# Optimization experiments

Measured on AMD Instinct MI355X. Metric: run time of the kernel, lower is better.

Reference implementation:

```python
import jax, jax.numpy as jnp
import numpy as np

EPS_LN = 1e-6
EPS_COS = 1e-8  # torch F.cosine_similarity default eps


def setup_inputs() -> dict:
    key = jax.random.key(0)
    ks = jax.random.split(key, 6)
    in_dim, hidden, out_dim, b = 1024, 512, 128, 8192
    x = jax.random.normal(ks[0], (b, in_dim), dtype=jnp.float32)
    # Linear layers: torch default init ~ U(-1/sqrt(fan_in), 1/sqrt(fan_in))
    w1 = jax.random.uniform(ks[1], (in_dim, hidden), jnp.float32, -1, 1) / np.sqrt(in_dim)
    b1 = jax.random.uniform(ks[2], (hidden,), jnp.float32, -1, 1) / np.sqrt(in_dim)
    w2 = jax.random.uniform(ks[3], (hidden, out_dim), jnp.float32, -1, 1) / np.sqrt(hidden)
    b2 = jax.random.uniform(ks[4], (out_dim,), jnp.float32, -1, 1) / np.sqrt(hidden)
    prelu_a = jnp.float32(0.25)  # nn.PReLU default: single shared parameter, init 0.25
    ln_gamma = jnp.ones((hidden,), jnp.float32)
    ln_beta = jnp.zeros((hidden,), jnp.float32)
    return {"x": x, "w1": w1, "b1": b1, "prelu_a": prelu_a,
            "ln_gamma": ln_gamma, "ln_beta": ln_beta, "w2": w2, "b2": b2}


def _layer_norm(h, gamma, beta):
    mu = jnp.mean(h, axis=-1, keepdims=True)
    var = jnp.mean(jnp.square(h - mu), axis=-1, keepdims=True)
    return (h - mu) * jax.lax.rsqrt(var + EPS_LN) * gamma + beta


def reference(x, w1, b1, prelu_a, ln_gamma, ln_beta, w2, b2):
    h = x @ w1 + b1                              # [b, hidden]
    h = jnp.where(h >= 0, h, prelu_a * h)        # PReLU
    h = _layer_norm(h, ln_gamma, ln_beta)        # Dropout is identity in reference
    z = h @ w2 + b2                              # [b, out_dim]
    # get_y_hat: full pairwise cosine similarity as normalize + Gram matmul
    norms = jnp.maximum(jnp.linalg.norm(z, axis=1, keepdims=True), EPS_COS)
    zn = z / norms                               # [b, out_dim]
    y_hat = zn @ zn.T                            # [b, b]
    return z, y_hat
```

## Files before the change

### kernel.cpp

```cpp
#include <hip/hip_runtime.h>
#include <stdint.h>

typedef uint16_t u16;
typedef __bf16 bf16x8 __attribute__((ext_vector_type(8)));
typedef float f32x4 __attribute__((ext_vector_type(4)));

__device__ __forceinline__ u16 f2bf(float f) {
  union { float f; uint32_t u; } v; v.f = f;
  uint32_t u = v.u;
  u += 0x7FFFu + ((u >> 16) & 1u);
  return (u16)(u >> 16);
}
__device__ __forceinline__ float bf2f(u16 h) {
  union { uint32_t u; float f; } v; v.u = ((uint32_t)h) << 16; return v.f;
}

__global__ void transpose_f32_to_bf16(const float* __restrict__ in,
                                      u16* __restrict__ out, int R, int C) {
  __shared__ float tile[32][33];
  int bx = blockIdx.x * 32, by = blockIdx.y * 32;
  int tx = threadIdx.x, ty = threadIdx.y;
  for (int i = 0; i < 32; i += 8)
    tile[ty + i][tx] = in[(size_t)(by + ty + i) * C + bx + tx];
  __syncthreads();
  for (int i = 0; i < 32; i += 8)
    out[(size_t)(bx + ty + i) * R + by + tx] = f2bf(tile[tx][ty + i]);
}

#define BM 128
#define BN 128
#define BKT 64

__launch_bounds__(256)
__global__ void gemm1_kernel(const float* __restrict__ A,
                             const u16* __restrict__ Bt,
                             const float* __restrict__ bias,
                             const float* __restrict__ prelu_a,
                             u16* __restrict__ out) {
  const int N = 512, K = 1024;
  __shared__ u16 As[BM][BKT + 8];
  __shared__ u16 Bs[BN][BKT + 8];
  const int lane = threadIdx.x & 63, wave = threadIdx.x >> 6;
  const int row0 = blockIdx.x * BM, col0 = blockIdx.y * BN;

  f32x4 zero4 = {0.f, 0.f, 0.f, 0.f};
  f32x4 acc[2][8];
  for (int i = 0; i < 2; ++i)
    for (int j = 0; j < 8; ++j) acc[i][j] = zero4;

  for (int k0 = 0; k0 < K; k0 += BKT) {
    for (int s = 0; s < 4; ++s) {
      int c = threadIdx.x + s * 256;
      int r = c >> 3, kc = (c & 7) << 3;
      const float4* p = (const float4*)(A + (size_t)(row0 + r) * K + k0 + kc);
      float4 f0 = p[0], f1 = p[1];
      u16 tmp[8] = {f2bf(f0.x), f2bf(f0.y), f2bf(f0.z), f2bf(f0.w),
                    f2bf(f1.x), f2bf(f1.y), f2bf(f1.z), f2bf(f1.w)};
      *(uint4*)(&As[r][kc]) = *(uint4*)tmp;
      *(uint4*)(&Bs[r][kc]) = *(const uint4*)(Bt + (size_t)(col0 + r) * K + k0 + kc);
    }
    __syncthreads();
    for (int kk = 0; kk < BKT; kk += 32) {
      bf16x8 a[2], b[8];
      for (int i = 0; i < 2; ++i)
        a[i] = *(const bf16x8*)(&As[wave * 32 + i * 16 + (lane & 15)][kk + (lane >> 4) * 8]);
      for (int j = 0; j < 8; ++j)
        b[j] = *(const bf16x8*)(&Bs[j * 16 + (lane & 15)][kk + (lane >> 4) * 8]);
      for (int i = 0; i < 2; ++i)
        for (int j = 0; j < 8; ++j)
          acc[i][j] = __builtin_amdgcn_mfma_f32_16x16x32_bf16(a[i], b[j], acc[i][j], 0, 0, 0);
    }
    __syncthreads();
  }

  float ap = *prelu_a;
  for (int i = 0; i < 2; ++i)
    for (int r = 0; r < 4; ++r) {
      int row = row0 + wave * 32 + i * 16 + (lane >> 4) * 4 + r;
      for (int j = 0; j < 8; ++j) {
        int col = col0 + j * 16 + (lane & 15);
        float v = acc[i][j][r] + bias[col];
        v = v >= 0.f ? v : ap * v;
        out[(size_t)row * N + col] = f2bf(v);
      }
    }
}

__launch_bounds__(256)
__global__ void ln_kernel(const u16* __restrict__ h, const float* __restrict__ gamma,
                          const float* __restrict__ beta, u16* __restrict__ out) {
  int lane = threadIdx.x & 63, wave = threadIdx.x >> 6;
  int row = blockIdx.x * 4 + wave;
  uint4 raw = *(const uint4*)(h + (size_t)row * 512 + lane * 8);
  u16* up = (u16*)&raw;
  float v[8], s = 0.f, s2 = 0.f;
  for (int e = 0; e < 8; ++e) { v[e] = bf2f(up[e]); s += v[e]; s2 += v[e] * v[e]; }
  for (int m = 1; m < 64; m <<= 1) { s += __shfl_xor(s, m); s2 += __shfl_xor(s2, m); }
  float mu = s * (1.f / 512.f);
  float var = s2 * (1.f / 512.f) - mu * mu;
  float rstd = rsqrtf(var + 1e-6f);
  u16 o[8];
  for (int e = 0; e < 8; ++e) {
    int c = lane * 8 + e;
    o[e] = f2bf((v[e] - mu) * rstd * gamma[c] + beta[c]);
  }
  *(uint4*)(out + (size_t)row * 512 + lane * 8) = *(uint4*)o;
}

__launch_bounds__(256)
__global__ void gemm2_kernel(const u16* __restrict__ A, const u16* __restrict__ Bt,
                             const float* __restrict__ bias,
                             float* __restrict__ z, u16* __restrict__ zn) {
  const int K = 512;
  __shared__ u16 As[BM][BKT + 8];
  __shared__ u16 Bs[BN][BKT + 8];
  const int lane = threadIdx.x & 63, wave = threadIdx.x >> 6;
  const int row0 = blockIdx.x * BM;

  f32x4 zero4 = {0.f, 0.f, 0.f, 0.f};
  f32x4 acc[2][8];
  for (int i = 0; i < 2; ++i)
    for (int j = 0; j < 8; ++j) acc[i][j] = zero4;

  for (int k0 = 0; k0 < K; k0 += BKT) {
    for (int s = 0; s < 4; ++s) {
      int c = threadIdx.x + s * 256;
      int r = c >> 3, kc = (c & 7) << 3;
      *(uint4*)(&As[r][kc]) = *(const uint4*)(A + (size_t)(row0 + r) * K + k0 + kc);
      *(uint4*)(&Bs[r][kc]) = *(const uint4*)(Bt + (size_t)r * K + k0 + kc);
    }
    __syncthreads();
    for (int kk = 0; kk < BKT; kk += 32) {
      bf16x8 a[2], b[8];
      for (int i = 0; i < 2; ++i)
        a[i] = *(const bf16x8*)(&As[wave * 32 + i * 16 + (lane & 15)][kk + (lane >> 4) * 8]);
      for (int j = 0; j < 8; ++j)
        b[j] = *(const bf16x8*)(&Bs[j * 16 + (lane & 15)][kk + (lane >> 4) * 8]);
      for (int i = 0; i < 2; ++i)
        for (int j = 0; j < 8; ++j)
          acc[i][j] = __builtin_amdgcn_mfma_f32_16x16x32_bf16(a[i], b[j], acc[i][j], 0, 0, 0);
    }
    __syncthreads();
  }

  for (int i = 0; i < 2; ++i)
    for (int r = 0; r < 4; ++r) {
      int row = row0 + wave * 32 + i * 16 + (lane >> 4) * 4 + r;
      float vv[8], s = 0.f;
      for (int j = 0; j < 8; ++j) {
        int col = j * 16 + (lane & 15);
        float v = acc[i][j][r] + bias[col];
        vv[j] = v; s += v * v;
      }
      s += __shfl_xor(s, 1); s += __shfl_xor(s, 2);
      s += __shfl_xor(s, 4); s += __shfl_xor(s, 8);
      float inv = 1.f / fmaxf(sqrtf(s), 1e-8f);
      for (int j = 0; j < 8; ++j) {
        int col = j * 16 + (lane & 15);
        z[(size_t)row * 128 + col] = vv[j];
        zn[(size_t)row * 128 + col] = f2bf(vv[j] * inv);
      }
    }
}

__launch_bounds__(256)
__global__ void gram_kernel(const u16* __restrict__ Z, float* __restrict__ y) {
  const int K = 128, Bdim = 8192;
  __shared__ u16 As[BM][BKT + 8];
  __shared__ u16 Bs[BN][BKT + 8];
  const int lane = threadIdx.x & 63, wave = threadIdx.x >> 6;
  const int row0 = blockIdx.x * BM, col0 = blockIdx.y * BN;

  f32x4 zero4 = {0.f, 0.f, 0.f, 0.f};
  f32x4 acc[2][8];
  for (int i = 0; i < 2; ++i)
    for (int j = 0; j < 8; ++j) acc[i][j] = zero4;

  for (int k0 = 0; k0 < K; k0 += BKT) {
    for (int s = 0; s < 4; ++s) {
      int c = threadIdx.x + s * 256;
      int r = c >> 3, kc = (c & 7) << 3;
      *(uint4*)(&As[r][kc]) = *(const uint4*)(Z + (size_t)(row0 + r) * K + k0 + kc);
      *(uint4*)(&Bs[r][kc]) = *(const uint4*)(Z + (size_t)(col0 + r) * K + k0 + kc);
    }
    __syncthreads();
    for (int kk = 0; kk < BKT; kk += 32) {
      bf16x8 a[2], b[8];
      for (int i = 0; i < 2; ++i)
        a[i] = *(const bf16x8*)(&As[wave * 32 + i * 16 + (lane & 15)][kk + (lane >> 4) * 8]);
      for (int j = 0; j < 8; ++j)
        b[j] = *(const bf16x8*)(&Bs[j * 16 + (lane & 15)][kk + (lane >> 4) * 8]);
      for (int i = 0; i < 2; ++i)
        for (int j = 0; j < 8; ++j)
          acc[i][j] = __builtin_amdgcn_mfma_f32_16x16x32_bf16(a[i], b[j], acc[i][j], 0, 0, 0);
    }
    __syncthreads();
  }

  for (int i = 0; i < 2; ++i)
    for (int r = 0; r < 4; ++r) {
      int row = row0 + wave * 32 + i * 16 + (lane >> 4) * 4 + r;
      for (int j = 0; j < 8; ++j) {
        int col = col0 + j * 16 + (lane & 15);
        y[(size_t)row * Bdim + col] = acc[i][j][r];
      }
    }
}

extern "C" void kernel_launch(void* const* d_in, const int* in_sizes, int n_in,
                              void* d_out, int out_size, void* d_ws, size_t ws_size,
                              hipStream_t stream) {
  const float* x       = (const float*)d_in[0];
  const float* w1      = (const float*)d_in[1];
  const float* b1      = (const float*)d_in[2];
  const float* prelu_a = (const float*)d_in[3];
  const float* gamma   = (const float*)d_in[4];
  const float* beta    = (const float*)d_in[5];
  const float* w2      = (const float*)d_in[6];
  const float* b2      = (const float*)d_in[7];

  float* z_out = (float*)d_out;
  float* yhat  = z_out + (size_t)8192 * 128;

  char* ws = (char*)d_ws;
  u16* w1t  = (u16*)(ws);
  u16* w2t  = (u16*)(ws + (1u << 20));
  u16* hact = (u16*)(ws + (1u << 20) + (1u << 17));
  u16* hln  = (u16*)(ws + (1u << 20) + (1u << 17) + (8u << 20));
  u16* zn   = (u16*)(ws + (1u << 20) + (1u << 17) + (16u << 20));

  transpose_f32_to_bf16<<<dim3(16, 32), dim3(32, 8), 0, stream>>>(w1, w1t, 1024, 512);
  transpose_f32_to_bf16<<<dim3(4, 16), dim3(32, 8), 0, stream>>>(w2, w2t, 512, 128);
  gemm1_kernel<<<dim3(64, 4), 256, 0, stream>>>(x, w1t, b1, prelu_a, hact);
  ln_kernel<<<2048, 256, 0, stream>>>(hact, gamma, beta, hln);
  gemm2_kernel<<<64, 256, 0, stream>>>(hln, w2t, b2, z_out, zn);
  gram_kernel<<<dim3(64, 64), 256, 0, stream>>>(zn, yhat);
}
```

Before: 367.6 us.

## Fuse LayerNorm into GEMM1, merge transposes, single-stage gram, nontemporal stores

Folds the LayerNorm into the first GEMM by giving each block 32 full rows across all 512 hidden columns and reducing row statistics through shared memory. This removes the intermediate activation round-trip and one launch. It also merges the two weight transposes into a single launch. The gram kernel now loads the whole K=128 slice at once, dropping its k-loop syncs, and the large y_hat and z outputs use nontemporal stores. GEMM1 now reloads all of W1 per 32-row block and uses a much larger shared tile, which may reduce occupancy.

```diff
diff --git a/kernel.cpp b/kernel.cpp
--- a/kernel.cpp
+++ b/kernel.cpp
@@ -15,8 +15,14 @@
   union { uint32_t u; float f; } v; v.u = ((uint32_t)h) << 16; return v.f;
 }
 
-__global__ void transpose_f32_to_bf16(const float* __restrict__ in,
-                                      u16* __restrict__ out, int R, int C) {
+__global__ void transpose_both(const float* __restrict__ w1, u16* __restrict__ w1t,
+                               const float* __restrict__ w2, u16* __restrict__ w2t) {
+  const float* in; u16* out; int R, C;
+  if (blockIdx.z == 0) { in = w1; out = w1t; R = 1024; C = 512; }
+  else {
+    if (blockIdx.x >= 4 || blockIdx.y >= 16) return;
+    in = w2; out = w2t; R = 512; C = 128;
+  }
   __shared__ float tile[32][33];
   int bx = blockIdx.x * 32, by = blockIdx.y * 32;
   int tx = threadIdx.x, ty = threadIdx.y;
@@ -27,85 +33,130 @@
     out[(size_t)(bx + ty + i) * R + by + tx] = f2bf(tile[tx][ty + i]);
 }
 
+#define G1_BK 64
+
+__launch_bounds__(256)
+__global__ void gemm1_ln_kernel(const float* __restrict__ A,
+                                const u16* __restrict__ Bt,
+                                const float* __restrict__ bias,
+                                const float* __restrict__ prelu_a,
+                                const float* __restrict__ gamma,
+                                const float* __restrict__ beta,
+                                u16* __restrict__ out) {
+  const int K = 1024, N = 512;
+  __shared__ u16 As[32][G1_BK + 8];
+  __shared__ u16 Bs[512][G1_BK + 8];
+  const int lane = threadIdx.x & 63, wave = threadIdx.x >> 6;
+  const int row0 = blockIdx.x * 32;
+
+  f32x4 zero4 = {0.f, 0.f, 0.f, 0.f};
+  f32x4 acc[2][8];
+#pragma unroll
+  for (int i = 0; i < 2; ++i)
+#pragma unroll
+    for (int j = 0; j < 8; ++j) acc[i][j] = zero4;
+
+  const int r0 = threadIdx.x >> 3, kc0 = (threadIdx.x & 7) << 3;
+
+  for (int k0 = 0; k0 < K; k0 += G1_BK) {
+    {
+      const float4* p = (const float4*)(A + (size_t)(row0 + r0) * K + k0 + kc0);
+      float4 f0 = p[0], f1 = p[1];
+      u16 tmp[8] = {f2bf(f0.x), f2bf(f0.y), f2bf(f0.z), f2bf(f0.w),
+                    f2bf(f1.x), f2bf(f1.y), f2bf(f1.z), f2bf(f1.w)};
+      *(uint4*)(&As[r0][kc0]) = *(uint4*)tmp;
+    }
+#pragma unroll
+    for (int s = 0; s < 16; ++s) {
+      int r = r0 + s * 32;
+      *(uint4*)(&Bs[r][kc0]) = *(const uint4*)(Bt + (size_t)r * K + k0 + kc0);
+    }
+    __syncthreads();
+#pragma unroll
+    for (int kk = 0; kk < G1_BK; kk += 32) {
+      bf16x8 a[2], b[8];
+#pragma unroll
+      for (int i = 0; i < 2; ++i)
+        a[i] = *(const bf16x8*)(&As[i * 16 + (lane & 15)][kk + (lane >> 4) * 8]);
+#pragma unroll
+      for (int j = 0; j < 8; ++j)
+        b[j] = *(const bf16x8*)(&Bs[wave * 128 + j * 16 + (lane & 15)][kk + (lane >> 4) * 8]);
+#pragma unroll
+      for (int i = 0; i < 2; ++i)
+#pragma unroll
+        for (int j = 0; j < 8; ++j)
+          acc[i][j] = __builtin_amdgcn_mfma_f32_16x16x32_bf16(a[i], b[j], acc[i][j], 0, 0, 0);
+    }
+    __syncthreads();
+  }
+
+  float ap = *prelu_a;
+  float bcol[8], gcol[8], btc[8];
+#pragma unroll
+  for (int j = 0; j < 8; ++j) {
+    int col = wave * 128 + j * 16 + (lane & 15);
+    bcol[j] = bias[col]; gcol[j] = gamma[col]; btc[j] = beta[col];
+  }
+
+  float s1[2][4], s2[2][4];
+#pragma unroll
+  for (int i = 0; i < 2; ++i)
+#pragma unroll
+    for (int r = 0; r < 4; ++r) {
+      float s = 0.f, q = 0.f;
+#pragma unroll
+      for (int j = 0; j < 8; ++j) {
+        float v = acc[i][j][r] + bcol[j];
+        v = v >= 0.f ? v : ap * v;
+        acc[i][j][r] = v;
+        s += v; q += v * v;
+      }
+      s += __shfl_xor(s, 1); q += __shfl_xor(q, 1);
+      s += __shfl_xor(s, 2); q += __shfl_xor(q, 2);
+      s += __shfl_xor(s, 4); q += __shfl_xor(q, 4);
+      s += __shfl_xor(s, 8); q += __shfl_xor(q, 8);
+      s1[i][r] = s; s2[i][r] = q;
+    }
+
+  float* red = (float*)&As[0][0];
+  if ((lane & 15) == 0) {
+#pragma unroll
+    for (int i = 0; i < 2; ++i)
+#pragma unroll
+      for (int r = 0; r < 4; ++r) {
+        int row = i * 16 + (lane >> 4) * 4 + r;
+        red[(row * 4 + wave) * 2 + 0] = s1[i][r];
+        red[(row * 4 + wave) * 2 + 1] = s2[i][r];
+      }
+  }
+  __syncthreads();
+
+#pragma unroll
+  for (int i = 0; i < 2; ++i)
+#pragma unroll
+    for (int r = 0; r < 4; ++r) {
+      int row = i * 16 + (lane >> 4) * 4 + r;
+      float S = 0.f, Q = 0.f;
+#pragma unroll
+      for (int w = 0; w < 4; ++w) {
+        S += red[(row * 4 + w) * 2 + 0];
+        Q += red[(row * 4 + w) * 2 + 1];
+      }
+      float mu = S * (1.f / 512.f);
+      float var = Q * (1.f / 512.f) - mu * mu;
+      float rstd = rsqrtf(var + 1e-6f);
+#pragma unroll
+      for (int j = 0; j < 8; ++j) {
+        int col = wave * 128 + j * 16 + (lane & 15);
+        out[(size_t)(row0 + row) * N + col] =
+            f2bf((acc[i][j][r] - mu) * rstd * gcol[j] + btc[j]);
+      }
+    }
+}
+
 #define BM 128
 #define BN 128
 #define BKT 64
-
-__launch_bounds__(256)
-__global__ void gemm1_kernel(const float* __restrict__ A,
-                             const u16* __restrict__ Bt,
-                             const float* __restrict__ bias,
-                             const float* __restrict__ prelu_a,
-                             u16* __restrict__ out) {
-  const int N = 512, K = 1024;
-  __shared__ u16 As[BM][BKT + 8];
-  __shared__ u16 Bs[BN][BKT + 8];
-  const int lane = threadIdx.x & 63, wave = threadIdx.x >> 6;
-  const int row0 = blockIdx.x * BM, col0 = blockIdx.y * BN;
-
-  f32x4 zero4 = {0.f, 0.f, 0.f, 0.f};
-  f32x4 acc[2][8];
-  for (int i = 0; i < 2; ++i)
-    for (int j = 0; j < 8; ++j) acc[i][j] = zero4;
-
-  for (int k0 = 0; k0 < K; k0 += BKT) {
-    for (int s = 0; s < 4; ++s) {
-      int c = threadIdx.x + s * 256;
-      int r = c >> 3, kc = (c & 7) << 3;
-      const float4* p = (const float4*)(A + (size_t)(row0 + r) * K + k0 + kc);
-      float4 f0 = p[0], f1 = p[1];
-      u16 tmp[8] = {f2bf(f0.x), f2bf(f0.y), f2bf(f0.z), f2bf(f0.w),
-                    f2bf(f1.x), f2bf(f1.y), f2bf(f1.z), f2bf(f1.w)};
-      *(uint4*)(&As[r][kc]) = *(uint4*)tmp;
-      *(uint4*)(&Bs[r][kc]) = *(const uint4*)(Bt + (size_t)(col0 + r) * K + k0 + kc);
-    }
-    __syncthreads();
-    for (int kk = 0; kk < BKT; kk += 32) {
-      bf16x8 a[2], b[8];
-      for (int i = 0; i < 2; ++i)
-        a[i] = *(const bf16x8*)(&As[wave * 32 + i * 16 + (lane & 15)][kk + (lane >> 4) * 8]);
-      for (int j = 0; j < 8; ++j)
-        b[j] = *(const bf16x8*)(&Bs[j * 16 + (lane & 15)][kk + (lane >> 4) * 8]);
-      for (int i = 0; i < 2; ++i)
-        for (int j = 0; j < 8; ++j)
-          acc[i][j] = __builtin_amdgcn_mfma_f32_16x16x32_bf16(a[i], b[j], acc[i][j], 0, 0, 0);
-    }
-    __syncthreads();
-  }
-
-  float ap = *prelu_a;
-  for (int i = 0; i < 2; ++i)
-    for (int r = 0; r < 4; ++r) {
-      int row = row0 + wave * 32 + i * 16 + (lane >> 4) * 4 + r;
-      for (int j = 0; j < 8; ++j) {
-        int col = col0 + j * 16 + (lane & 15);
-        float v = acc[i][j][r] + bias[col];
-        v = v >= 0.f ? v : ap * v;
-        out[(size_t)row * N + col] = f2bf(v);
-      }
-    }
-}
-
-__launch_bounds__(256)
-__global__ void ln_kernel(const u16* __restrict__ h, const float* __restrict__ gamma,
-                          const float* __restrict__ beta, u16* __restrict__ out) {
-  int lane = threadIdx.x & 63, wave = threadIdx.x >> 6;
-  int row = blockIdx.x * 4 + wave;
-  uint4 raw = *(const uint4*)(h + (size_t)row * 512 + lane * 8);
-  u16* up = (u16*)&raw;
-  float v[8], s = 0.f, s2 = 0.f;
-  for (int e = 0; e < 8; ++e) { v[e] = bf2f(up[e]); s += v[e]; s2 += v[e] * v[e]; }
-  for (int m = 1; m < 64; m <<= 1) { s += __shfl_xor(s, m); s2 += __shfl_xor(s2, m); }
-  float mu = s * (1.f / 512.f);
-  float var = s2 * (1.f / 512.f) - mu * mu;
-  float rstd = rsqrtf(var + 1e-6f);
-  u16 o[8];
-  for (int e = 0; e < 8; ++e) {
-    int c = lane * 8 + e;
-    o[e] = f2bf((v[e] - mu) * rstd * gamma[c] + beta[c]);
-  }
-  *(uint4*)(out + (size_t)row * 512 + lane * 8) = *(uint4*)o;
-}
 
 __launch_bounds__(256)
 __global__ void gemm2_kernel(const u16* __restrict__ A, const u16* __restrict__ Bt,
@@ -119,34 +170,46 @@
 
   f32x4 zero4 = {0.f, 0.f, 0.f, 0.f};
   f32x4 acc[2][8];
-  for (int i = 0; i < 2; ++i)
+#pragma unroll
+  for (int i = 0; i < 2; ++i)
+#pragma unroll
     for (int j = 0; j < 8; ++j) acc[i][j] = zero4;
 
+  const int r0 = threadIdx.x >> 3, kc0 = (threadIdx.x & 7) << 3;
+
   for (int k0 = 0; k0 < K; k0 += BKT) {
+#pragma unroll
     for (int s = 0; s < 4; ++s) {
-      int c = threadIdx.x + s * 256;
-      int r = c >> 3, kc = (c & 7) << 3;
-      *(uint4*)(&As[r][kc]) = *(const uint4*)(A + (size_t)(row0 + r) * K + k0 + kc);
-      *(uint4*)(&Bs[r][kc]) = *(const uint4*)(Bt + (size_t)r * K + k0 + kc);
+      int r = r0 + s * 32;
+      *(uint4*)(&As[r][kc0]) = *(const uint4*)(A + (size_t)(row0 + r) * K + k0 + kc0);
+      *(uint4*)(&Bs[r][kc0]) = *(const uint4*)(Bt + (size_t)r * K + k0 + kc0);
     }
     __syncthreads();
+#pragma unroll
     for (int kk = 0; kk < BKT; kk += 32) {
       bf16x8 a[2], b[8];
+#pragma unroll
       for (int i = 0; i < 2; ++i)
         a[i] = *(const bf16x8*)(&As[wave * 32 + i * 16 + (lane & 15)][kk + (lane >> 4) * 8]);
+#pragma unroll
       for (int j = 0; j < 8; ++j)
         b[j] = *(const bf16x8*)(&Bs[j * 16 + (lane & 15)][kk + (lane >> 4) * 8]);
+#pragma unroll
       for (int i = 0; i < 2; ++i)
+#pragma unroll
         for (int j = 0; j < 8; ++j)
           acc[i][j] = __builtin_amdgcn_mfma_f32_16x16x32_bf16(a[i], b[j], acc[i][j], 0, 0, 0);
     }
     __syncthreads();
   }
 
-  for (int i = 0; i < 2; ++i)
+#pragma unroll
+  for (int i = 0; i < 2; ++i)
+#pragma unroll
     for (int r = 0; r < 4; ++r) {
       int row = row0 + wave * 32 + i * 16 + (lane >> 4) * 4 + r;
       float vv[8], s = 0.f;
+#pragma unroll
       for (int j = 0; j < 8; ++j) {
         int col = j * 16 + (lane & 15);
         float v = acc[i][j][r] + bias[col];
@@ -155,9 +218,10 @@
       s += __shfl_xor(s, 1); s += __shfl_xor(s, 2);
       s += __shfl_xor(s, 4); s += __shfl_xor(s, 8);
       float inv = 1.f / fmaxf(sqrtf(s), 1e-8f);
+#pragma unroll
       for (int j = 0; j < 8; ++j) {
         int col = j * 16 + (lane & 15);
-        z[(size_t)row * 128 + col] = vv[j];
+        __builtin_nontemporal_store(vv[j], &z[(size_t)row * 128 + col]);
         zn[(size_t)row * 128 + col] = f2bf(vv[j] * inv);
       }
     }
@@ -166,43 +230,52 @@
 __launch_bounds__(256)
 __global__ void gram_kernel(const u16* __restrict__ Z, float* __restrict__ y) {
   const int K = 128, Bdim = 8192;
-  __shared__ u16 As[BM][BKT + 8];
-  __shared__ u16 Bs[BN][BKT + 8];
+  __shared__ u16 As[128][K + 8];
+  __shared__ u16 Bs[128][K + 8];
   const int lane = threadIdx.x & 63, wave = threadIdx.x >> 6;
-  const int row0 = blockIdx.x * BM, col0 = blockIdx.y * BN;
+  const int row0 = blockIdx.x * 128, col0 = blockIdx.y * 128;
 
   f32x4 zero4 = {0.f, 0.f, 0.f, 0.f};
   f32x4 acc[2][8];
-  for (int i = 0; i < 2; ++i)
+#pragma unroll
+  for (int i = 0; i < 2; ++i)
+#pragma unroll
     for (int j = 0; j < 8; ++j) acc[i][j] = zero4;
 
-  for (int k0 = 0; k0 < K; k0 += BKT) {
-    for (int s = 0; s < 4; ++s) {
-      int c = threadIdx.x + s * 256;
-      int r = c >> 3, kc = (c & 7) << 3;
-      *(uint4*)(&As[r][kc]) = *(const uint4*)(Z + (size_t)(row0 + r) * K + k0 + kc);
-      *(uint4*)(&Bs[r][kc]) = *(const uint4*)(Z + (size_t)(col0 + r) * K + k0 + kc);
-    }
-    __syncthreads();
-    for (int kk = 0; kk < BKT; kk += 32) {
-      bf16x8 a[2], b[8];
-      for (int i = 0; i < 2; ++i)
-        a[i] = *(const bf16x8*)(&As[wave * 32 + i * 16 + (lane & 15)][kk + (lane >> 4) * 8]);
+  const int r0 = threadIdx.x >> 4, kc0 = (threadIdx.x & 15) << 3;
+#pragma unroll
+  for (int s = 0; s < 8; ++s) {
+    int r = r0 + s * 16;
+    *(uint4*)(&As[r][kc0]) = *(const uint4*)(Z + (size_t)(row0 + r) * K + kc0);
+    *(uint4*)(&Bs[r][kc0]) = *(const uint4*)(Z + (size_t)(col0 + r) * K + kc0);
+  }
+  __syncthreads();
+
+#pragma unroll
+  for (int kk = 0; kk < K; kk += 32) {
+    bf16x8 a[2], b[8];
+#pragma unroll
+    for (int i = 0; i < 2; ++i)
+      a[i] = *(const bf16x8*)(&As[wave * 32 + i * 16 + (lane & 15)][kk + (lane >> 4) * 8]);
+#pragma unroll
+    for (int j = 0; j < 8; ++j)
+      b[j] = *(const bf16x8*)(&Bs[j * 16 + (lane & 15)][kk + (lane >> 4) * 8]);
+#pragma unroll
+    for (int i = 0; i < 2; ++i)
+#pragma unroll
       for (int j = 0; j < 8; ++j)
-        b[j] = *(const bf16x8*)(&Bs[j * 16 + (lane & 15)][kk + (lane >> 4) * 8]);
-      for (int i = 0; i < 2; ++i)
-        for (int j = 0; j < 8; ++j)
-          acc[i][j] = __builtin_amdgcn_mfma_f32_16x16x32_bf16(a[i], b[j], acc[i][j], 0, 0, 0);
-    }
-    __syncthreads();
-  }
-
-  for (int i = 0; i < 2; ++i)
+        acc[i][j] = __builtin_amdgcn_mfma_f32_16x16x32_bf16(a[i], b[j], acc[i][j], 0, 0, 0);
+  }
+
+#pragma unroll
+  for (int i = 0; i < 2; ++i)
+#pragma unroll
     for (int r = 0; r < 4; ++r) {
       int row = row0 + wave * 32 + i * 16 + (lane >> 4) * 4 + r;
+#pragma unroll
       for (int j = 0; j < 8; ++j) {
         int col = col0 + j * 16 + (lane & 15);
-        y[(size_t)row * Bdim + col] = acc[i][j][r];
+        __builtin_nontemporal_store(acc[i][j][r], &y[(size_t)row * Bdim + col]);
       }
     }
 }
@@ -223,16 +296,13 @@
   float* yhat  = z_out + (size_t)8192 * 128;
 
   char* ws = (char*)d_ws;
-  u16* w1t  = (u16*)(ws);
-  u16* w2t  = (u16*)(ws + (1u << 20));
-  u16* hact = (u16*)(ws + (1u << 20) + (1u << 17));
-  u16* hln  = (u16*)(ws + (1u << 20) + (1u << 17) + (8u << 20));
-  u16* zn   = (u16*)(ws + (1u << 20) + (1u << 17) + (16u << 20));
-
-  transpose_f32_to_bf16<<<dim3(16, 32), dim3(32, 8), 0, stream>>>(w1, w1t, 1024, 512);
-  transpose_f32_to_bf16<<<dim3(4, 16), dim3(32, 8), 0, stream>>>(w2, w2t, 512, 128);
-  gemm1_kernel<<<dim3(64, 4), 256, 0, stream>>>(x, w1t, b1, prelu_a, hact);
-  ln_kernel<<<2048, 256, 0, stream>>>(hact, gamma, beta, hln);
+  u16* w1t = (u16*)(ws);
+  u16* w2t = (u16*)(ws + (1u << 20));
+  u16* hln = (u16*)(ws + (1u << 20) + (1u << 17));
+  u16* zn  = (u16*)(ws + (1u << 20) + (1u << 17) + (8u << 20));
+
+  transpose_both<<<dim3(16, 32, 2), dim3(32, 8), 0, stream>>>(w1, w1t, w2, w2t);
+  gemm1_ln_kernel<<<256, 256, 0, stream>>>(x, w1t, b1, prelu_a, gamma, beta, hln);
   gemm2_kernel<<<64, 256, 0, stream>>>(hln, w2t, b2, z_out, zn);
   gram_kernel<<<dim3(64, 64), 256, 0, stream>>>(zn, yhat);
 }
```

Result: slower. 384.3 us (+4.5%).

## Merge weight transposes, load full K in gram, add nontemporal stores and unrolls

Applied to the files above, without the earlier changes.

Merges the two weight-transpose launches into one grid using blockIdx.z, which removes a kernel launch. The gram kernel now loads the whole K=128 slice into shared memory in one pass with a single barrier instead of two staged iterations. Its output writes and the z writes in gemm2 become nontemporal stores, aimed at the 256MB y_hat write that dominates traffic. Explicit unroll pragmas are added throughout. The larger shared tiles in gram (about 68KB per block) may reduce occupancy.

```diff
diff --git a/kernel.cpp b/kernel.cpp
--- a/kernel.cpp
+++ b/kernel.cpp
@@ -15,8 +15,14 @@
   union { uint32_t u; float f; } v; v.u = ((uint32_t)h) << 16; return v.f;
 }
 
-__global__ void transpose_f32_to_bf16(const float* __restrict__ in,
-                                      u16* __restrict__ out, int R, int C) {
+__global__ void transpose_both(const float* __restrict__ w1, u16* __restrict__ w1t,
+                               const float* __restrict__ w2, u16* __restrict__ w2t) {
+  const float* in; u16* out; int R, C;
+  if (blockIdx.z == 0) { in = w1; out = w1t; R = 1024; C = 512; }
+  else {
+    if (blockIdx.x >= 4 || blockIdx.y >= 16) return;
+    in = w2; out = w2t; R = 512; C = 128;
+  }
   __shared__ float tile[32][33];
   int bx = blockIdx.x * 32, by = blockIdx.y * 32;
   int tx = threadIdx.x, ty = threadIdx.y;
@@ -45,10 +51,13 @@
 
   f32x4 zero4 = {0.f, 0.f, 0.f, 0.f};
   f32x4 acc[2][8];
-  for (int i = 0; i < 2; ++i)
+#pragma unroll
+  for (int i = 0; i < 2; ++i)
+#pragma unroll
     for (int j = 0; j < 8; ++j) acc[i][j] = zero4;
 
   for (int k0 = 0; k0 < K; k0 += BKT) {
+#pragma unroll
     for (int s = 0; s < 4; ++s) {
       int c = threadIdx.x + s * 256;
       int r = c >> 3, kc = (c & 7) << 3;
@@ -60,13 +69,18 @@
       *(uint4*)(&Bs[r][kc]) = *(const uint4*)(Bt + (size_t)(col0 + r) * K + k0 + kc);
     }
     __syncthreads();
+#pragma unroll
     for (int kk = 0; kk < BKT; kk += 32) {
       bf16x8 a[2], b[8];
+#pragma unroll
       for (int i = 0; i < 2; ++i)
         a[i] = *(const bf16x8*)(&As[wave * 32 + i * 16 + (lane & 15)][kk + (lane >> 4) * 8]);
+#pragma unroll
       for (int j = 0; j < 8; ++j)
         b[j] = *(const bf16x8*)(&Bs[j * 16 + (lane & 15)][kk + (lane >> 4) * 8]);
-      for (int i = 0; i < 2; ++i)
+#pragma unroll
+      for (int i = 0; i < 2; ++i)
+#pragma unroll
         for (int j = 0; j < 8; ++j)
           acc[i][j] = __builtin_amdgcn_mfma_f32_16x16x32_bf16(a[i], b[j], acc[i][j], 0, 0, 0);
     }
@@ -74,9 +88,12 @@
   }
 
   float ap = *prelu_a;
-  for (int i = 0; i < 2; ++i)
+#pragma unroll
+  for (int i = 0; i < 2; ++i)
+#pragma unroll
     for (int r = 0; r < 4; ++r) {
       int row = row0 + wave * 32 + i * 16 + (lane >> 4) * 4 + r;
+#pragma unroll
       for (int j = 0; j < 8; ++j) {
         int col = col0 + j * 16 + (lane & 15);
         float v = acc[i][j][r] + bias[col];
@@ -94,12 +111,14 @@
   uint4 raw = *(const uint4*)(h + (size_t)row * 512 + lane * 8);
   u16* up = (u16*)&raw;
   float v[8], s = 0.f, s2 = 0.f;
+#pragma unroll
   for (int e = 0; e < 8; ++e) { v[e] = bf2f(up[e]); s += v[e]; s2 += v[e] * v[e]; }
   for (int m = 1; m < 64; m <<= 1) { s += __shfl_xor(s, m); s2 += __shfl_xor(s2, m); }
   float mu = s * (1.f / 512.f);
   float var = s2 * (1.f / 512.f) - mu * mu;
   float rstd = rsqrtf(var + 1e-6f);
   u16 o[8];
+#pragma unroll
   for (int e = 0; e < 8; ++e) {
     int c = lane * 8 + e;
     o[e] = f2bf((v[e] - mu) * rstd * gamma[c] + beta[c]);
@@ -119,34 +138,46 @@
 
   f32x4 zero4 = {0.f, 0.f, 0.f, 0.f};
   f32x4 acc[2][8];
-  for (int i = 0; i < 2; ++i)
+#pragma unroll
+  for (int i = 0; i < 2; ++i)
+#pragma unroll
     for (int j = 0; j < 8; ++j) acc[i][j] = zero4;
 
+  const int r0 = threadIdx.x >> 3, kc0 = (threadIdx.x & 7) << 3;
+
   for (int k0 = 0; k0 < K; k0 += BKT) {
+#pragma unroll
     for (int s = 0; s < 4; ++s) {
-      int c = threadIdx.x + s * 256;
-      int r = c >> 3, kc = (c & 7) << 3;
-      *(uint4*)(&As[r][kc]) = *(const uint4*)(A + (size_t)(row0 + r) * K + k0 + kc);
-      *(uint4*)(&Bs[r][kc]) = *(const uint4*)(Bt + (size_t)r * K + k0 + kc);
-    }
-    __syncthreads();
+      int r = r0 + s * 32;
+      *(uint4*)(&As[r][kc0]) = *(const uint4*)(A + (size_t)(row0 + r) * K + k0 + kc0);
+      *(uint4*)(&Bs[r][kc0]) = *(const uint4*)(Bt + (size_t)r * K + k0 + kc0);
+    }
+    __syncthreads();
+#pragma unroll
     for (int kk = 0; kk < BKT; kk += 32) {
       bf16x8 a[2], b[8];
+#pragma unroll
       for (int i = 0; i < 2; ++i)
         a[i] = *(const bf16x8*)(&As[wave * 32 + i * 16 + (lane & 15)][kk + (lane >> 4) * 8]);
+#pragma unroll
       for (int j = 0; j < 8; ++j)
         b[j] = *(const bf16x8*)(&Bs[j * 16 + (lane & 15)][kk + (lane >> 4) * 8]);
-      for (int i = 0; i < 2; ++i)
+#pragma unroll
+      for (int i = 0; i < 2; ++i)
+#pragma unroll
         for (int j = 0; j < 8; ++j)
           acc[i][j] = __builtin_amdgcn_mfma_f32_16x16x32_bf16(a[i], b[j], acc[i][j], 0, 0, 0);
     }
     __syncthreads();
   }
 
-  for (int i = 0; i < 2; ++i)
+#pragma unroll
+  for (int i = 0; i < 2; ++i)
+#pragma unroll
     for (int r = 0; r < 4; ++r) {
       int row = row0 + wave * 32 + i * 16 + (lane >> 4) * 4 + r;
       float vv[8], s = 0.f;
+#pragma unroll
       for (int j = 0; j < 8; ++j) {
         int col = j * 16 + (lane & 15);
         float v = acc[i][j][r] + bias[col];
@@ -155,9 +186,10 @@
       s += __shfl_xor(s, 1); s += __shfl_xor(s, 2);
       s += __shfl_xor(s, 4); s += __shfl_xor(s, 8);
       float inv = 1.f / fmaxf(sqrtf(s), 1e-8f);
+#pragma unroll
       for (int j = 0; j < 8; ++j) {
         int col = j * 16 + (lane & 15);
-        z[(size_t)row * 128 + col] = vv[j];
+        __builtin_nontemporal_store(vv[j], &z[(size_t)row * 128 + col]);
         zn[(size_t)row * 128 + col] = f2bf(vv[j] * inv);
       }
     }
@@ -166,43 +198,52 @@
 __launch_bounds__(256)
 __global__ void gram_kernel(const u16* __restrict__ Z, float* __restrict__ y) {
   const int K = 128, Bdim = 8192;
-  __shared__ u16 As[BM][BKT + 8];
-  __shared__ u16 Bs[BN][BKT + 8];
+  __shared__ u16 As[128][K + 8];
+  __shared__ u16 Bs[128][K + 8];
   const int lane = threadIdx.x & 63, wave = threadIdx.x >> 6;
-  const int row0 = blockIdx.x * BM, col0 = blockIdx.y * BN;
+  const int row0 = blockIdx.x * 128, col0 = blockIdx.y * 128;
 
   f32x4 zero4 = {0.f, 0.f, 0.f, 0.f};
   f32x4 acc[2][8];
-  for (int i = 0; i < 2; ++i)
+#pragma unroll
+  for (int i = 0; i < 2; ++i)
+#pragma unroll
     for (int j = 0; j < 8; ++j) acc[i][j] = zero4;
 
-  for (int k0 = 0; k0 < K; k0 += BKT) {
-    for (int s = 0; s < 4; ++s) {
-      int c = threadIdx.x + s * 256;
-      int r = c >> 3, kc = (c & 7) << 3;
-      *(uint4*)(&As[r][kc]) = *(const uint4*)(Z + (size_t)(row0 + r) * K + k0 + kc);
-      *(uint4*)(&Bs[r][kc]) = *(const uint4*)(Z + (size_t)(col0 + r) * K + k0 + kc);
-    }
-    __syncthreads();
-    for (int kk = 0; kk < BKT; kk += 32) {
-      bf16x8 a[2], b[8];
-      for (int i = 0; i < 2; ++i)
-        a[i] = *(const bf16x8*)(&As[wave * 32 + i * 16 + (lane & 15)][kk + (lane >> 4) * 8]);
+  const int r0 = threadIdx.x >> 4, kc0 = (threadIdx.x & 15) << 3;
+#pragma unroll
+  for (int s = 0; s < 8; ++s) {
+    int r = r0 + s * 16;
+    *(uint4*)(&As[r][kc0]) = *(const uint4*)(Z + (size_t)(row0 + r) * K + kc0);
+    *(uint4*)(&Bs[r][kc0]) = *(const uint4*)(Z + (size_t)(col0 + r) * K + kc0);
+  }
+  __syncthreads();
+
+#pragma unroll
+  for (int kk = 0; kk < K; kk += 32) {
+    bf16x8 a[2], b[8];
+#pragma unroll
+    for (int i = 0; i < 2; ++i)
+      a[i] = *(const bf16x8*)(&As[wave * 32 + i * 16 + (lane & 15)][kk + (lane >> 4) * 8]);
+#pragma unroll
+    for (int j = 0; j < 8; ++j)
+      b[j] = *(const bf16x8*)(&Bs[j * 16 + (lane & 15)][kk + (lane >> 4) * 8]);
+#pragma unroll
+    for (int i = 0; i < 2; ++i)
+#pragma unroll
       for (int j = 0; j < 8; ++j)
-        b[j] = *(const bf16x8*)(&Bs[j * 16 + (lane & 15)][kk + (lane >> 4) * 8]);
-      for (int i = 0; i < 2; ++i)
-        for (int j = 0; j < 8; ++j)
-          acc[i][j] = __builtin_amdgcn_mfma_f32_16x16x32_bf16(a[i], b[j], acc[i][j], 0, 0, 0);
-    }
-    __syncthreads();
-  }
-
-  for (int i = 0; i < 2; ++i)
+        acc[i][j] = __builtin_amdgcn_mfma_f32_16x16x32_bf16(a[i], b[j], acc[i][j], 0, 0, 0);
+  }
+
+#pragma unroll
+  for (int i = 0; i < 2; ++i)
+#pragma unroll
     for (int r = 0; r < 4; ++r) {
       int row = row0 + wave * 32 + i * 16 + (lane >> 4) * 4 + r;
+#pragma unroll
       for (int j = 0; j < 8; ++j) {
         int col = col0 + j * 16 + (lane & 15);
-        y[(size_t)row * Bdim + col] = acc[i][j][r];
+        __builtin_nontemporal_store(acc[i][j][r], &y[(size_t)row * Bdim + col]);
       }
     }
 }
@@ -229,8 +270,7 @@
   u16* hln  = (u16*)(ws + (1u << 20) + (1u << 17) + (8u << 20));
   u16* zn   = (u16*)(ws + (1u << 20) + (1u << 17) + (16u << 20));
 
-  transpose_f32_to_bf16<<<dim3(16, 32), dim3(32, 8), 0, stream>>>(w1, w1t, 1024, 512);
-  transpose_f32_to_bf16<<<dim3(4, 16), dim3(32, 8), 0, stream>>>(w2, w2t, 512, 128);
+  transpose_both<<<dim3(16, 32, 2), dim3(32, 8), 0, stream>>>(w1, w1t, w2, w2t);
   gemm1_kernel<<<dim3(64, 4), 256, 0, stream>>>(x, w1t, b1, prelu_a, hact);
   ln_kernel<<<2048, 256, 0, stream>>>(hact, gamma, beta, hln);
   gemm2_kernel<<<64, 256, 0, stream>>>(hln, w2t, b2, z_out, zn);
```

Result: slower. 386.4 us (+5.1%).
